# Kernel optimization log

Hardware: AMD Instinct MI355X
Metric: run time of the kernel (lower is better)

The kernel has to match this reference:

```python
import jax, jax.numpy as jnp
import numpy as np

NEG = jnp.float32(-1e30)   # stand-in for -inf (keeps grads NaN-free)
DUP = jnp.float32(-2e30)   # mask for duplicate (merged-away) candidates


def ctc_prefix_beam_search(logits, beam_size, blank_index):
    """Vectorized CTC prefix beam search, faithful to the torch `beams` fn.
    Prefixes are fixed-length int32 token arrays padded with -1 (bijective
    encoding of the original strings since alphabet chars are unique).
    Returns (scores=[B] logaddexp(pb,pnb), prefixes=[B,T], lengths=[B])."""
    T, V = logits.shape
    B = beam_size
    K = beam_size  # torch code takes top-beam_size symbols per frame
    ctc = jax.nn.log_softmax(logits, axis=-1)  # [T,V] log-probs
    pos = jnp.arange(T)

    # initial beam: one empty hypothesis, rest are -inf dummies with unique
    # sentinel first tokens so they never merge with real prefixes
    prefixes = jnp.full((B, T), -1, jnp.int32)
    sent = -(jnp.arange(B, dtype=jnp.int32) + 2)
    prefixes = prefixes.at[:, 0].set(jnp.where(jnp.arange(B) == 0, -1, sent))
    lengths = jnp.zeros((B,), jnp.int32)
    pb = jnp.full((B,), NEG, jnp.float32).at[0].set(0.0)   # ends-in-blank logp
    pnb = jnp.full((B,), NEG, jnp.float32)                 # ends-in-nonblank logp

    def step(carry, logp):
        prefixes, lengths, pb, pnb = carry
        ps, s = jax.lax.top_k(logp, K)                     # [K] values, indices
        is_blank = (s == blank_index)[None, :]             # [1,K]
        last = jnp.where(lengths > 0,
                         prefixes[jnp.arange(B), jnp.maximum(lengths - 1, 0)],
                         -1)                               # [B] last token or -1
        same = last[:, None] == s[None, :]                 # [B,K]
        pb_ps = pb[:, None] + ps[None, :]
        pnb_ps = pnb[:, None] + ps[None, :]
        both = jnp.logaddexp(pb_ps, pnb_ps)

        # group 1: prefix unchanged (blank emission, or repeat of last symbol)
        g1_pb = jnp.where(is_blank, both, NEG)
        g1_pnb = jnp.where(same & ~is_blank, pnb_ps, NEG)
        g1_prefix = jnp.broadcast_to(prefixes[:, None, :], (B, K, T))
        g1_len = jnp.broadcast_to(lengths[:, None], (B, K))

        # group 2: prefix extended by s (non-blank only; blank rows get NEG)
        g2_pnb = jnp.where(is_blank, NEG, jnp.where(same, pb_ps, both))
        g2_pb = jnp.full((B, K), NEG, jnp.float32)
        g2_prefix = jnp.where(pos[None, None, :] == lengths[:, None, None],
                              s[None, :, None], prefixes[:, None, :])
        g2_len = g1_len + 1

        C = 2 * B * K
        cand_prefix = jnp.concatenate([g1_prefix, g2_prefix]).reshape(C, T)
        cand_len = jnp.concatenate([g1_len, g2_len]).reshape(C)
        cand_pb = jnp.concatenate([g1_pb, g2_pb]).reshape(C)
        cand_pnb = jnp.concatenate([g1_pnb, g2_pnb]).reshape(C)

        # merge candidates with identical prefixes (the dict logsumexp in torch)
        eq = jnp.all(cand_prefix[:, None, :] == cand_prefix[None, :, :], axis=-1)
        merged_pb = jax.nn.logsumexp(jnp.where(eq, cand_pb[None, :], NEG), axis=1)
        merged_pnb = jax.nn.logsumexp(jnp.where(eq, cand_pnb[None, :], NEG), axis=1)
        first = jnp.argmax(eq, axis=1) == jnp.arange(C)    # keep first occurrence
        total = jnp.logaddexp(merged_pb, merged_pnb)
        _, idx = jax.lax.top_k(jnp.where(first, total, DUP), B)

        return (cand_prefix[idx], cand_len[idx], merged_pb[idx], merged_pnb[idx]), None

    (prefixes, lengths, pb, pnb), _ = jax.lax.scan(
        step, (prefixes, lengths, pb, pnb), ctc)
    scores = jnp.logaddexp(pb, pnb)
    return scores, prefixes, lengths


def setup_inputs() -> dict:
    key = jax.random.key(0)
    T, V = 200, 29
    logits = jax.random.normal(key, (T, V), dtype=jnp.float32)
    return {"logits": logits, "beam_size": 10, "blank_index": 28}


def reference(logits, beam_size, blank_index):
    return ctc_prefix_beam_search(logits, beam_size, blank_index)
```

## Files before the change

kernel.cpp:

```cpp
#include <hip/hip_runtime.h>
#include <math.h>


#define BB 10
#define KK 10
#define VV 29
#define TMAX 256
#define FS 56
#define NEGF (-1e30f)
#define DUPF (-2e30f)
#define MAGICF 0x5CA7F00Du
#define SENTB 0x7F800000

__device__ __forceinline__ float lae(float a, float b) {
    float m = fmaxf(a, b);
    return m + log1pf(expf(fminf(a, b) - m));
}
__device__ __forceinline__ unsigned int ordf(float f) {
    unsigned int u = __float_as_uint(f);
    return (u & 0x80000000u) ? ~u : (u | 0x80000000u);
}

__device__ __forceinline__ void topk_frame(const float* __restrict__ logits,
                                           int blank, int t, float* __restrict__ o,
                                           int L) {
    float lp = (L < VV) ? logits[t * VV + L] : -INFINITY;
    float mx = lp;
    #pragma unroll
    for (int off = 32; off >= 1; off >>= 1) mx = fmaxf(mx, __shfl_xor(mx, off));
    float sm = (L < VV) ? expf(lp - mx) : 0.f;
    #pragma unroll
    for (int off = 32; off >= 1; off >>= 1) sm += __shfl_xor(sm, off);
    float lz = mx + logf(sm);
    int arank = 0;
    #pragma unroll
    for (int u = 0; u < VV; ++u) {
        float lu = __shfl(lp, u);
        arank += (lu > lp) || (lu == lp && u < L);
    }
    bool win = (L < VV) && (arank < KK);
    if (win) { o[2 * arank] = __int_as_float(L); o[2 * arank + 1] = lp - lz; }
    if (L < 32) o[24 + L] = win ? (lp - lz) : __int_as_float(SENTB);
    unsigned long long bm = __ballot(win && (L == blank));
    if (bm) { if (L == blank) { o[20] = __int_as_float(arank); o[21] = lp - lz; } }
    else    { if (L == 0)     { o[20] = __int_as_float(-1);    o[21] = 0.f;     } }
}

__global__ __launch_bounds__(128) void fused_kernel(
        const float* __restrict__ logits, const int* __restrict__ blank_p,
        float* __restrict__ out, int T, float* __restrict__ tkbuf,
        unsigned int* fflags) {

    const int L = threadIdx.x;

    if (blockIdx.x != 0) {
        const int t = blockIdx.x - 1;
        if (L < 64) topk_frame(logits, blank_p[0], t, tkbuf + t * FS, L);
        __syncthreads();
        if (L == 0)
            __hip_atomic_store(&fflags[t], MAGICF, __ATOMIC_RELEASE,
                               __HIP_MEMORY_SCOPE_AGENT);
        return;
    }

    __shared__ __align__(16) float tkl[TMAX * FS];
    __shared__ __align__(16) float bsrow[16][8];
    __shared__ __align__(16) int   dupsig[12];
    __shared__ __align__(16) unsigned long long kbuf[128];
    __shared__ __align__(16) float4 aux4[12];
    __shared__ unsigned short hist[TMAX][BB];
    __shared__ signed char pout[BB][TMAX];

    if (L < BB) {
        int last0 = (L == 0) ? -1 : -(L + 2);
        int par0  = (L == 0) ? -1 : 0;
        int f2 = (last0 + 16) | ((par0 + 1) << 8) | ((-1 + 16) << 16);
        *(float4*)&bsrow[L][0] = make_float4((L == 0) ? 0.f : NEGF, NEGF,
                                             __int_as_float(f2), __int_as_float(0));
        *(float4*)&bsrow[L][4] = make_float4(0.f, NEGF, __int_as_float(SENTB), 0.f);
        dupsig[L] = f2 & 0xFFFF;
    } else if (L < 12) dupsig[L] = 0;

    if (L < 64) {
        for (;;) {
            bool ok = true;
            for (int base = 0; base < T; base += 64) {
                int idx = base + L;
                unsigned f = (idx < T)
                    ? __hip_atomic_load(&fflags[idx], __ATOMIC_RELAXED,
                                        __HIP_MEMORY_SCOPE_AGENT)
                    : MAGICF;
                ok = ok && (f == MAGICF);
            }
            if (__all(ok)) break;
        }
    }
    __syncthreads();
    __builtin_amdgcn_fence(__ATOMIC_ACQUIRE, "agent");

    {
        int n4 = (T * FS) >> 2;
        const float4* g4 = (const float4*)tkbuf;
        float4* l4 = (float4*)tkl;
        for (int i = L; i < n4; i += 128) l4[i] = g4[i];
    }
    __syncthreads();

    const int c = L;
    const bool active = c < BB + BB * KK;
    const bool isg1 = c < BB;
    const bool isshadow = (L >= 110 && L < 120);
    const int b = isg1 ? c : (c - 10) / 10;
    const int k = isg1 ? 0 : (c - 10) % 10;
    const int ofs = isg1 ? 20 : 2 * k;
    const int blank = blank_p[0];

    float2 fpr = *(const float2*)&tkl[ofs];

    for (int t = 0; t < T; ++t) {
        float tot = -INFINITY, pay_pb = NEGF, pay_pnb = NEGF;
        int nlen = 0, nlast = 0, xsl = -1, tok = -1;

        if (active) {
            float4 rowA = *(const float4*)&bsrow[b][0];
            int f2 = __float_as_int(rowA.z);
            int last_b = (f2 & 255) - 16;
            if (isg1) {
                float4 rowB = *(const float4*)&bsrow[b][4];
                int par_b  = ((f2 >> 8) & 255) - 1;
                int last_p = ((f2 >> 16) & 255) - 16;
                nlen = __float_as_int(rowA.w);
                nlast = last_b; xsl = par_b; tok = -1;
                int bk = __float_as_int(fpr.x);
                float pbl = fpr.y;
                float pkl = rowB.z;
                if (bk >= 0) pay_pb = lae(rowA.x + pbl, rowA.y + pbl);
                if (__float_as_int(rowB.z) != SENTB) {
                    float a = rowA.y + pkl;
                    if (par_b >= 0) {
                        float e = (last_b == last_p) ? (rowB.x + pkl)
                                   : lae(rowB.x + pkl, rowB.y + pkl);
                        float mxx = fmaxf(a, e);
                        pay_pnb = mxx + logf(expf(a - mxx) + expf(e - mxx));
                    } else pay_pnb = a;
                }
                tot = lae(pay_pb, pay_pnb);
            } else {
                int s = __float_as_int(fpr.x); float p = fpr.y;
                nlen = __float_as_int(rowA.w) + 1;
                nlast = s; xsl = b; tok = s;
                int4 dg0 = *(const int4*)&dupsig[0];
                int4 dg1 = *(const int4*)&dupsig[4];
                int2 dg2 = *(const int2*)&dupsig[8];
                int sig[BB] = {dg0.x, dg0.y, dg0.z, dg0.w,
                               dg1.x, dg1.y, dg1.z, dg1.w, dg2.x, dg2.y};
                int target = ((b + 1) << 8) | (s + 16);
                bool dup = false;
                #pragma unroll
                for (int i = 0; i < BB; ++i) dup = dup || (sig[i] == target);
                float v;
                if (s == blank)        v = NEGF;
                else if (s == last_b)  v = rowA.x + p;
                else                   v = lae(rowA.x + p, rowA.y + p);
                pay_pnb = v;
                tot = dup ? DUPF : v;
            }
        }

        unsigned long long key =
            (((unsigned long long)ordf(tot)) << 32) | (unsigned)(127 - c);
        if (active) kbuf[c] = key;
        if (isg1)   aux4[c] = make_float4(pay_pb, pay_pnb,
                                          __int_as_float(nlast + 16), 0.f);
        __syncthreads();

        if (isshadow) key = kbuf[L - 110];

        int tn = (t + 1 < T) ? (t + 1) : t;
        const float* tkn = &tkl[tn * FS];
        fpr = *(const float2*)&tkn[ofs];

        int r = 0;
        const ulonglong2* k2 = (const ulonglong2*)kbuf;
        #pragma unroll
        for (int q = 0; q < 55; ++q) {
            ulonglong2 w = k2[q];
            r += (w.x > key) + (w.y > key);
        }

        int g1r_val = ((isg1 || isshadow) && r < BB) ? r : -1;
        int xs = (xsl < 0) ? 0 : xsl;
        int src = (L < 64) ? xs : (46 + xs);
        int g1r_sh = __shfl(g1r_val, src);

        if (active && r < BB) {
            float4 ax = aux4[xs];
            int npar, plast16; float ppb, ppnb;
            if (xsl >= 0) {
                npar = g1r_sh; plast16 = __float_as_int(ax.z);
                ppb = ax.x; ppnb = ax.y;
            } else { npar = -1; plast16 = 15; ppb = 0.f; ppnb = NEGF; }
            int li = ((unsigned)nlast < VV) ? nlast : 29;
            float npkl = tkn[24 + li];
            int f2n = (nlast + 16) | ((npar + 1) << 8) | (plast16 << 16);
            *(float4*)&bsrow[r][0] = make_float4(isg1 ? pay_pb : NEGF, pay_pnb,
                                                 __int_as_float(f2n),
                                                 __int_as_float(nlen));
            *(float4*)&bsrow[r][4] = make_float4(ppb, ppnb, npkl, 0.f);
            dupsig[r] = f2n & 0xFFFF;
            hist[t][r] = (unsigned short)(b | ((tok + 1) << 8));
        }
        __syncthreads();
    }

    int mylen = 0;
    if (L < BB) {
        float4 rj = *(const float4*)&bsrow[L][0];
        mylen = __float_as_int(rj.w);
        out[L] = lae(rj.x, rj.y);
        out[BB + BB * T + L] = (float)mylen;
    }
    for (int i = L; i < BB * TMAX; i += 128) (&pout[0][0])[i] = -1;
    __syncthreads();
    if (L < BB) {
        int cur = L, pos = mylen - 1;
        for (int tt = T - 1; tt >= 0; --tt) {
            unsigned short h = hist[tt][cur];
            int tk2 = (h >> 8) - 1;
            if (tk2 >= 0) pout[L][pos--] = (signed char)tk2;
            cur = h & 255;
        }
        if (mylen == 0 && cur > 0) pout[L][0] = (signed char)(-(cur + 2));
    }
    __syncthreads();
    for (int e = L; e < BB * T; e += 128) {
        int j = e / T, p = e - j * T;
        out[BB + e] = (float)pout[j][p];
    }
}

extern "C" void kernel_launch(void* const* d_in, const int* in_sizes, int n_in,
                              void* d_out, int out_size, void* d_ws, size_t ws_size,
                              hipStream_t stream) {
    const float* logits = (const float*)d_in[0];
    const int* blank_p = (const int*)d_in[2];
    int T = in_sizes[0] / VV;
    float* tkbuf = (float*)d_ws;

    size_t ff_off = ((size_t)T * FS * 4 + 255) & ~(size_t)255;
    unsigned int* fflags = (unsigned int*)((char*)d_ws + ff_off);

    fused_kernel<<<dim3(1 + T), dim3(128), 0, stream>>>(
        logits, blank_p, (float*)d_out, T, tkbuf, fflags);
}
```

Measured before the change: 527.6 us.

## Run beam-search loop in a single wavefront, replacing barriers with waitcnt

The sequential per-frame beam loop now runs on one 64-lane wavefront, with each lane handling two candidates instead of spreading 110 candidates over two wavefronts. The block-wide __syncthreads barriers inside the time loop are replaced by an lgkmcnt wait, relying on lockstep execution within a single wave. This removes two barriers per frame in exchange for doubling per-lane compare work in the rank computation. It depends on wave64 lockstep semantics for correctness of the LDS communication.

```diff
diff --git a/kernel.cpp b/kernel.cpp
--- a/kernel.cpp
+++ b/kernel.cpp
@@ -11,6 +11,8 @@
 #define DUPF (-2e30f)
 #define MAGICF 0x5CA7F00Du
 #define SENTB 0x7F800000
+
+#define WSYNC() asm volatile("s_waitcnt lgkmcnt(0)" ::: "memory")
 
 __device__ __forceinline__ float lae(float a, float b) {
     float m = fmaxf(a, b);
@@ -69,7 +71,7 @@
     __shared__ __align__(16) unsigned long long kbuf[128];
     __shared__ __align__(16) float4 aux4[12];
     __shared__ unsigned short hist[TMAX][BB];
-    __shared__ signed char pout[BB][TMAX];
+    __shared__ __align__(16) signed char pout[BB][TMAX];
 
     if (L < BB) {
         int last0 = (L == 0) ? -1 : -(L + 2);
@@ -105,112 +107,158 @@
         for (int i = L; i < n4; i += 128) l4[i] = g4[i];
     }
     __syncthreads();
-
-    const int c = L;
-    const bool active = c < BB + BB * KK;
-    const bool isg1 = c < BB;
-    const bool isshadow = (L >= 110 && L < 120);
-    const int b = isg1 ? c : (c - 10) / 10;
-    const int k = isg1 ? 0 : (c - 10) % 10;
-    const int ofs = isg1 ? 20 : 2 * k;
+    if (L >= 64) return;
+
+    const int c0 = L;
+    const bool g1_0 = (c0 < BB);
+    const int b0 = g1_0 ? c0 : (c0 - 10) / 10;
+    const int k0 = g1_0 ? 0 : (c0 - 10) % 10;
+    const int ofs0 = g1_0 ? 20 : 2 * k0;
+    const bool has1 = (L < BB * KK - 64 + 10);
+    const int c1 = 64 + L;
+    const int b1 = (c1 - 10) / 10;
+    const int k1 = (c1 - 10) % 10;
+    const int ofs1 = 2 * k1;
     const int blank = blank_p[0];
 
-    float2 fpr = *(const float2*)&tkl[ofs];
+    float2 fpr0 = *(const float2*)&tkl[ofs0];
+    float2 fpr1 = *(const float2*)&tkl[ofs1];
 
     for (int t = 0; t < T; ++t) {
-        float tot = -INFINITY, pay_pb = NEGF, pay_pnb = NEGF;
-        int nlen = 0, nlast = 0, xsl = -1, tok = -1;
-
-        if (active) {
-            float4 rowA = *(const float4*)&bsrow[b][0];
-            int f2 = __float_as_int(rowA.z);
-            int last_b = (f2 & 255) - 16;
-            if (isg1) {
-                float4 rowB = *(const float4*)&bsrow[b][4];
-                int par_b  = ((f2 >> 8) & 255) - 1;
-                int last_p = ((f2 >> 16) & 255) - 16;
-                nlen = __float_as_int(rowA.w);
-                nlast = last_b; xsl = par_b; tok = -1;
-                int bk = __float_as_int(fpr.x);
-                float pbl = fpr.y;
+        int4 dg0 = *(const int4*)&dupsig[0];
+        int4 dg1 = *(const int4*)&dupsig[4];
+        int2 dg2 = *(const int2*)&dupsig[8];
+        int sig[BB] = {dg0.x, dg0.y, dg0.z, dg0.w,
+                       dg1.x, dg1.y, dg1.z, dg1.w, dg2.x, dg2.y};
+
+        float4 rowA0 = *(const float4*)&bsrow[b0][0];
+        float4 rowA1 = *(const float4*)&bsrow[b1][0];
+
+        float tot0 = -INFINITY, pay_pb0 = NEGF, pay_pnb0 = NEGF;
+        int nlen0 = 0, nlast0 = 0, xsl0 = -1, tok0 = -1;
+        {
+            int f2_0 = __float_as_int(rowA0.z);
+            int last_b0 = (f2_0 & 255) - 16;
+            if (g1_0) {
+                float4 rowB = *(const float4*)&bsrow[b0][4];
+                int par_b  = ((f2_0 >> 8) & 255) - 1;
+                int last_p = ((f2_0 >> 16) & 255) - 16;
+                nlen0 = __float_as_int(rowA0.w);
+                nlast0 = last_b0; xsl0 = par_b; tok0 = -1;
+                int bk = __float_as_int(fpr0.x);
+                float pbl = fpr0.y;
                 float pkl = rowB.z;
-                if (bk >= 0) pay_pb = lae(rowA.x + pbl, rowA.y + pbl);
+                if (bk >= 0) pay_pb0 = lae(rowA0.x + pbl, rowA0.y + pbl);
                 if (__float_as_int(rowB.z) != SENTB) {
-                    float a = rowA.y + pkl;
+                    float a = rowA0.y + pkl;
                     if (par_b >= 0) {
-                        float e = (last_b == last_p) ? (rowB.x + pkl)
+                        float e = (last_b0 == last_p) ? (rowB.x + pkl)
                                    : lae(rowB.x + pkl, rowB.y + pkl);
                         float mxx = fmaxf(a, e);
-                        pay_pnb = mxx + logf(expf(a - mxx) + expf(e - mxx));
-                    } else pay_pnb = a;
+                        pay_pnb0 = mxx + logf(expf(a - mxx) + expf(e - mxx));
+                    } else pay_pnb0 = a;
                 }
-                tot = lae(pay_pb, pay_pnb);
+                tot0 = lae(pay_pb0, pay_pnb0);
             } else {
-                int s = __float_as_int(fpr.x); float p = fpr.y;
-                nlen = __float_as_int(rowA.w) + 1;
-                nlast = s; xsl = b; tok = s;
-                int4 dg0 = *(const int4*)&dupsig[0];
-                int4 dg1 = *(const int4*)&dupsig[4];
-                int2 dg2 = *(const int2*)&dupsig[8];
-                int sig[BB] = {dg0.x, dg0.y, dg0.z, dg0.w,
-                               dg1.x, dg1.y, dg1.z, dg1.w, dg2.x, dg2.y};
-                int target = ((b + 1) << 8) | (s + 16);
+                int s = __float_as_int(fpr0.x); float p = fpr0.y;
+                nlen0 = __float_as_int(rowA0.w) + 1;
+                nlast0 = s; xsl0 = b0; tok0 = s;
+                int target = ((b0 + 1) << 8) | (s + 16);
                 bool dup = false;
                 #pragma unroll
                 for (int i = 0; i < BB; ++i) dup = dup || (sig[i] == target);
                 float v;
                 if (s == blank)        v = NEGF;
-                else if (s == last_b)  v = rowA.x + p;
-                else                   v = lae(rowA.x + p, rowA.y + p);
-                pay_pnb = v;
-                tot = dup ? DUPF : v;
+                else if (s == last_b0) v = rowA0.x + p;
+                else                   v = lae(rowA0.x + p, rowA0.y + p);
+                pay_pnb0 = v;
+                tot0 = dup ? DUPF : v;
             }
         }
 
-        unsigned long long key =
-            (((unsigned long long)ordf(tot)) << 32) | (unsigned)(127 - c);
-        if (active) kbuf[c] = key;
-        if (isg1)   aux4[c] = make_float4(pay_pb, pay_pnb,
-                                          __int_as_float(nlast + 16), 0.f);
-        __syncthreads();
-
-        if (isshadow) key = kbuf[L - 110];
+        float tot1 = -INFINITY, pay_pnb1 = NEGF;
+        int nlen1 = 0, nlast1 = 0, tok1 = -1;
+        if (has1) {
+            int f2_1 = __float_as_int(rowA1.z);
+            int last_b1 = (f2_1 & 255) - 16;
+            int s = __float_as_int(fpr1.x); float p = fpr1.y;
+            nlen1 = __float_as_int(rowA1.w) + 1;
+            nlast1 = s; tok1 = s;
+            int target = ((b1 + 1) << 8) | (s + 16);
+            bool dup = false;
+            #pragma unroll
+            for (int i = 0; i < BB; ++i) dup = dup || (sig[i] == target);
+            float v;
+            if (s == blank)        v = NEGF;
+            else if (s == last_b1) v = rowA1.x + p;
+            else                   v = lae(rowA1.x + p, rowA1.y + p);
+            pay_pnb1 = v;
+            tot1 = dup ? DUPF : v;
+        }
+
+        unsigned long long key0 =
+            (((unsigned long long)ordf(tot0)) << 32) | (unsigned)(127 - c0);
+        unsigned long long key1 =
+            (((unsigned long long)ordf(tot1)) << 32) | (unsigned)(127 - c1);
+        kbuf[c0] = key0;
+        if (has1) kbuf[c1] = key1;
+        if (g1_0) aux4[c0] = make_float4(pay_pb0, pay_pnb0,
+                                         __int_as_float(nlast0 + 16), 0.f);
+        WSYNC();
 
         int tn = (t + 1 < T) ? (t + 1) : t;
         const float* tkn = &tkl[tn * FS];
-        fpr = *(const float2*)&tkn[ofs];
-
-        int r = 0;
+        fpr0 = *(const float2*)&tkn[ofs0];
+        fpr1 = *(const float2*)&tkn[ofs1];
+
+        int r0a = 0, r0b = 0, r1a = 0, r1b = 0;
         const ulonglong2* k2 = (const ulonglong2*)kbuf;
         #pragma unroll
         for (int q = 0; q < 55; ++q) {
             ulonglong2 w = k2[q];
-            r += (w.x > key) + (w.y > key);
-        }
-
-        int g1r_val = ((isg1 || isshadow) && r < BB) ? r : -1;
-        int xs = (xsl < 0) ? 0 : xsl;
-        int src = (L < 64) ? xs : (46 + xs);
-        int g1r_sh = __shfl(g1r_val, src);
-
-        if (active && r < BB) {
-            float4 ax = aux4[xs];
+            r0a += (w.x > key0); r0b += (w.y > key0);
+            r1a += (w.x > key1); r1b += (w.y > key1);
+        }
+        int r0 = r0a + r0b;
+        int r1 = r1a + r1b;
+
+        int g1r_val = (g1_0 && r0 < BB) ? r0 : -1;
+        int xs0 = g1_0 ? ((xsl0 < 0) ? 0 : xsl0) : b0;
+        int sh0 = __shfl(g1r_val, xs0);
+        int sh1 = __shfl(g1r_val, (b1 < BB) ? b1 : 0);
+
+        if (r0 < BB) {
+            float4 ax = aux4[xs0];
             int npar, plast16; float ppb, ppnb;
-            if (xsl >= 0) {
-                npar = g1r_sh; plast16 = __float_as_int(ax.z);
+            if (xsl0 >= 0) {
+                npar = sh0; plast16 = __float_as_int(ax.z);
                 ppb = ax.x; ppnb = ax.y;
             } else { npar = -1; plast16 = 15; ppb = 0.f; ppnb = NEGF; }
-            int li = ((unsigned)nlast < VV) ? nlast : 29;
+            int li = ((unsigned)nlast0 < VV) ? nlast0 : 29;
             float npkl = tkn[24 + li];
-            int f2n = (nlast + 16) | ((npar + 1) << 8) | (plast16 << 16);
-            *(float4*)&bsrow[r][0] = make_float4(isg1 ? pay_pb : NEGF, pay_pnb,
-                                                 __int_as_float(f2n),
-                                                 __int_as_float(nlen));
-            *(float4*)&bsrow[r][4] = make_float4(ppb, ppnb, npkl, 0.f);
-            dupsig[r] = f2n & 0xFFFF;
-            hist[t][r] = (unsigned short)(b | ((tok + 1) << 8));
-        }
-        __syncthreads();
+            int f2n = (nlast0 + 16) | ((npar + 1) << 8) | (plast16 << 16);
+            *(float4*)&bsrow[r0][0] = make_float4(g1_0 ? pay_pb0 : NEGF, pay_pnb0,
+                                                  __int_as_float(f2n),
+                                                  __int_as_float(nlen0));
+            *(float4*)&bsrow[r0][4] = make_float4(ppb, ppnb, npkl, 0.f);
+            dupsig[r0] = f2n & 0xFFFF;
+            hist[t][r0] = (unsigned short)(b0 | ((tok0 + 1) << 8));
+        }
+        if (has1 && r1 < BB) {
+            float4 ax = aux4[b1];
+            int npar = sh1, plast16 = __float_as_int(ax.z);
+            float ppb = ax.x, ppnb = ax.y;
+            int li = ((unsigned)nlast1 < VV) ? nlast1 : 29;
+            float npkl = tkn[24 + li];
+            int f2n = (nlast1 + 16) | ((npar + 1) << 8) | (plast16 << 16);
+            *(float4*)&bsrow[r1][0] = make_float4(NEGF, pay_pnb1,
+                                                  __int_as_float(f2n),
+                                                  __int_as_float(nlen1));
+            *(float4*)&bsrow[r1][4] = make_float4(ppb, ppnb, npkl, 0.f);
+            dupsig[r1] = f2n & 0xFFFF;
+            hist[t][r1] = (unsigned short)(b1 | ((tok1 + 1) << 8));
+        }
+        WSYNC();
     }
 
     int mylen = 0;
@@ -220,8 +268,8 @@
         out[L] = lae(rj.x, rj.y);
         out[BB + BB * T + L] = (float)mylen;
     }
-    for (int i = L; i < BB * TMAX; i += 128) (&pout[0][0])[i] = -1;
-    __syncthreads();
+    for (int i = L; i < BB * TMAX; i += 64) (&pout[0][0])[i] = -1;
+    WSYNC();
     if (L < BB) {
         int cur = L, pos = mylen - 1;
         for (int tt = T - 1; tt >= 0; --tt) {
@@ -232,8 +280,8 @@
         }
         if (mylen == 0 && cur > 0) pout[L][0] = (signed char)(-(cur + 2));
     }
-    __syncthreads();
-    for (int e = L; e < BB * T; e += 128) {
+    WSYNC();
+    for (int e = L; e < BB * T; e += 64) {
         int j = e / T, p = e - j * T;
         out[BB + e] = (float)pout[j][p];
     }
```

New measurement: 783.9 us. 48.6% more time.
